# Performance work log

Measured on AMD Instinct MI355X. Metric: run time of the kernel, lower is better.

## Reference

```python
import jax, jax.numpy as jnp
import numpy as np

B, M, C, D, H, W = 2, 4, 32, 32, 32, 32
E, O = 4, 128
MC = M * C
BN_EPS = 1e-5


def setup_inputs() -> dict:
    key = jax.random.key(0)
    ks = jax.random.split(key, 8)
    inp = {
        "f0": jax.random.normal(ks[0], (B, C, D, H, W), jnp.float32),
        "f1": jax.random.normal(ks[1], (B, C, D, H, W), jnp.float32),
        "f2": jax.random.normal(ks[2], (B, C, D, H, W), jnp.float32),
        "f3": jax.random.normal(ks[3], (B, C, D, H, W), jnp.float32),
        # per-expert 1x1x1 conv weights [E, O, MC] (bias=False)
        "Wc": jax.random.normal(ks[4], (E, O, MC), jnp.float32) * 0.05,
        # BatchNorm3d params (eval mode), per expert per out-channel
        "gamma": jnp.ones((E, O), jnp.float32),
        "beta": jnp.zeros((E, O), jnp.float32),
        "rmean": jnp.zeros((E, O), jnp.float32),
        "rvar": jnp.ones((E, O), jnp.float32),
        # router Linear(MC -> E)
        "Wr": jax.random.normal(ks[5], (E, MC), jnp.float32) * 0.02,
        "br": jnp.zeros((E,), jnp.float32),
        "top_k": 2,
    }
    return inp


def reference(f0, f1, f2, f3, Wc, gamma, beta, rmean, rvar, Wr, br, top_k):
    x = jnp.concatenate([f0, f1, f2, f3], axis=1)          # [B, MC, D, H, W]
    Bn, MCn, Dn, Hn, Wn = x.shape
    En = Wr.shape[0]

    # router: global average pool -> linear -> softmax -> top-k
    pooled = x.mean(axis=(2, 3, 4))                        # [B, MC]
    logits = pooled @ Wr.T + br                            # [B, E]
    probs = jax.nn.softmax(logits, axis=-1)
    topk_vals, topk_idx = jax.lax.top_k(probs, top_k)      # [B, k]
    topk_w = topk_vals / topk_vals.sum(axis=-1, keepdims=True)

    # auxiliary load-balancing loss (top-1 one-hot)
    one_hot = jax.nn.one_hot(topk_idx[:, 0], En, dtype=probs.dtype)
    f_e = one_hot.mean(axis=0)
    p_e = probs.mean(axis=0)
    aux_loss = En * (f_e * p_e).sum()

    # all experts: 1x1x1 conv == channel GEMM, then eval-mode BN + ReLU
    xs = x.reshape(Bn, MCn, -1)                            # [B, MC, S]
    y = jnp.einsum('eoc,bcs->ebos', Wc, xs)                # [E, B, O, S]
    inv = gamma * jax.lax.rsqrt(rvar + BN_EPS)             # [E, O]
    y = y * inv[:, None, :, None] + (beta - rmean * inv)[:, None, :, None]
    y = jax.nn.relu(y)

    # dispatch/combine: per-sample expert weights scattered to [B, E]
    cw = jnp.zeros((Bn, En), x.dtype).at[
        jnp.arange(Bn)[:, None], topk_idx
    ].add(topk_w)
    out = jnp.einsum('be,ebos->bos', cw, y).reshape(Bn, -1, Dn, Hn, Wn)
    return out, aux_loss
```

## Files before the change

### kernel.cpp

```cpp
#include <hip/hip_runtime.h>
#include <stdint.h>

#define S_TOT 32768
#define MC_DIM 128
#define O_DIM 128
#define BN_EPS 1e-5f
#define S_TILE 128

#define WS_PART  0
#define WS_BIAS  512
#define WS_W2    1024

typedef __attribute__((ext_vector_type(8))) short short8;
typedef __attribute__((ext_vector_type(4))) float f32x4;

static __device__ __forceinline__ unsigned short f2bf(float f) {
    union { float f; unsigned int u; } v; v.f = f;
    unsigned int r = v.u + 0x7FFFu + ((v.u >> 16) & 1u);
    return (unsigned short)(r >> 16);
}

__global__ __launch_bounds__(256) void k_pool(
    const float* __restrict__ f0, const float* __restrict__ f1,
    const float* __restrict__ f2, const float* __restrict__ f3,
    const float* __restrict__ Wc, const float* __restrict__ gamma,
    const float* __restrict__ beta, const float* __restrict__ rmean,
    const float* __restrict__ rvar, float* __restrict__ ws) {

    __shared__ float red[4];
    int bid = blockIdx.x;
    int half = bid >> 8, ch = bid & 255;
    int b = ch >> 7, c = ch & 127;
    int t = threadIdx.x;
    int wv = t >> 6, l = t & 63;

    if (t < 32) {
        int i = bid * 32 + t;
        int eo = i >> 5;
        float inv = gamma[eo] * rsqrtf(rvar[eo] + BN_EPS);
        float4 w = ((const float4*)Wc)[i];
        uint2 pk;
        pk.x = (unsigned int)f2bf(w.x * inv) | ((unsigned int)f2bf(w.y * inv) << 16);
        pk.y = (unsigned int)f2bf(w.z * inv) | ((unsigned int)f2bf(w.w * inv) << 16);
        ((uint2*)(ws + WS_W2))[i] = pk;
    } else if (t == 32) {
        float inv = gamma[bid] * rsqrtf(rvar[bid] + BN_EPS);
        ws[WS_BIAS + bid] = beta[bid] - rmean[bid] * inv;
    }

    const float* fp = (c < 32) ? f0 : (c < 64) ? f1 : (c < 96) ? f2 : f3;
    const float4* base = (const float4*)(fp + ((size_t)b * 32 + (c & 31)) * S_TOT + half * 16384);
    float s = 0.f;
    #pragma unroll
    for (int j = 0; j < 16; ++j) {
        float4 v = base[j * 256 + t];
        s += (v.x + v.y) + (v.z + v.w);
    }
    #pragma unroll
    for (int msk = 32; msk >= 1; msk >>= 1) s += __shfl_xor(s, msk);
    if (l == 0) red[wv] = s;
    __syncthreads();
    if (t == 0) ws[WS_PART + half * 256 + ch] = (red[0] + red[1]) + (red[2] + red[3]);
}

__global__ __launch_bounds__(256, 2) void k_moe(
    const float* __restrict__ f0, const float* __restrict__ f1,
    const float* __restrict__ f2, const float* __restrict__ f3,
    const float* __restrict__ Wr, const float* __restrict__ br,
    const float* __restrict__ ws, float* __restrict__ out) {

    __shared__ uint4 tile4[2048];
    __shared__ float pooled[256];
    __shared__ int   route_e[2];
    __shared__ float route_w[2];
    char* lds = (char*)tile4;

    int bid = blockIdx.x;
    int b = bid >> 8;
    int st = bid & 255;
    int s0 = st * S_TILE;
    int t = threadIdx.x;
    int wv = t >> 6, l = t & 63;

    #pragma unroll
    for (int m = 0; m < 4; ++m) {
        const float* fp = (m == 0) ? f0 : (m == 1) ? f1 : (m == 2) ? f2 : f3;
        #pragma unroll
        for (int it = 0; it < 4; ++it) {
            int lin = it * 256 + t;
            int cql = lin >> 7;
            int sl = lin & 127;
            const float* src = fp + ((size_t)b * 32 + cql * 4) * S_TOT + s0 + sl;
            float v0 = src[0];
            float v1 = src[S_TOT];
            float v2 = src[2 * (size_t)S_TOT];
            float v3 = src[3 * (size_t)S_TOT];
            int cq = m * 8 + cql;
            int gr = cq >> 1, half = cq & 1;
            int gswz = gr ^ (sl & 15);
            int byte = sl * 256 + gswz * 16 + half * 8;
            uint2 pk;
            pk.x = (unsigned int)f2bf(v0) | ((unsigned int)f2bf(v1) << 16);
            pk.y = (unsigned int)f2bf(v2) | ((unsigned int)f2bf(v3) << 16);
            *(uint2*)(lds + byte) = pk;
        }
    }

    pooled[t] = ws[WS_PART + t] + ws[WS_PART + 256 + t];
    __syncthreads();
    if (t < 64) {
        const float s_inv = 1.0f / (float)S_TOT;
        float x0 = pooled[l] * s_inv;
        float x1 = pooled[64 + l] * s_inv;
        float y0 = pooled[128 + l] * s_inv;
        float y1 = pooled[192 + l] * s_inv;
        float lg[8];
        #pragma unroll
        for (int e = 0; e < 4; ++e) {
            float wc0 = Wr[e * MC_DIM + l];
            float wc1 = Wr[e * MC_DIM + 64 + l];
            lg[e] = x0 * wc0 + x1 * wc1;
            lg[4 + e] = y0 * wc0 + y1 * wc1;
        }
        #pragma unroll
        for (int msk = 32; msk >= 1; msk >>= 1) {
            #pragma unroll
            for (int e = 0; e < 8; ++e) lg[e] += __shfl_xor(lg[e], msk);
        }
        if (l == 0) {
            float probs[2][4];
            int top1[2];
            #pragma unroll
            for (int bb = 0; bb < 2; ++bb) {
                float lo[4];
                for (int e = 0; e < 4; ++e) lo[e] = lg[bb * 4 + e] + br[e];
                float mx = fmaxf(fmaxf(lo[0], lo[1]), fmaxf(lo[2], lo[3]));
                float sum = 0.f;
                for (int e = 0; e < 4; ++e) { probs[bb][e] = expf(lo[e] - mx); sum += probs[bb][e]; }
                for (int e = 0; e < 4; ++e) probs[bb][e] /= sum;
                int e0 = 0; float v0 = probs[bb][0];
                for (int e = 1; e < 4; ++e) if (probs[bb][e] > v0) { v0 = probs[bb][e]; e0 = e; }
                int e1 = -1; float v1 = -1.f;
                for (int e = 0; e < 4; ++e) if (e != e0 && probs[bb][e] > v1) { v1 = probs[bb][e]; e1 = e; }
                top1[bb] = e0;
                if (bb == b) {
                    float inv = 1.f / (v0 + v1);
                    route_e[0] = e0; route_e[1] = e1;
                    route_w[0] = v0 * inv; route_w[1] = v1 * inv;
                }
            }
            if (bid == 0) {
                float aux = 0.f;
                for (int e = 0; e < 4; ++e) {
                    float fe = 0.5f * ((top1[0] == e) + (top1[1] == e));
                    float pe = 0.5f * (probs[0][e] + probs[1][e]);
                    aux += fe * pe;
                }
                out[(size_t)8388608] = 4.f * aux;
            }
        }
    }
    __syncthreads();

    int e0 = route_e[0], e1 = route_e[1];
    float w0 = route_w[0], w1 = route_w[1];
    const unsigned short* W2 = (const unsigned short*)(ws + WS_W2);
    const float* bias2 = ws + WS_BIAS;

    int o0 = wv * 32;
    int lr = l & 15, lg2 = l >> 4;

    f32x4 acc[2][2][8];
    #pragma unroll
    for (int ee = 0; ee < 2; ++ee)
        #pragma unroll
        for (int of = 0; of < 2; ++of)
            #pragma unroll
            for (int sf = 0; sf < 8; ++sf)
                acc[ee][of][sf] = (f32x4){0.f, 0.f, 0.f, 0.f};

    #pragma unroll
    for (int kk = 0; kk < 4; ++kk) {
        short8 a[2][2];
        #pragma unroll
        for (int ee = 0; ee < 2; ++ee) {
            int e = ee ? e1 : e0;
            #pragma unroll
            for (int of = 0; of < 2; ++of) {
                int o = o0 + of * 16 + lr;
                a[ee][of] = *(const short8*)(W2 + ((size_t)(e * O_DIM + o) * MC_DIM + kk * 32 + lg2 * 8));
            }
        }
        #pragma unroll
        for (int sf = 0; sf < 8; ++sf) {
            int sl = sf * 16 + lr;
            int gr = kk * 4 + lg2;
            int byte = sl * 256 + ((gr ^ lr) << 4);
            short8 bb = *(const short8*)(lds + byte);
            #pragma unroll
            for (int ee = 0; ee < 2; ++ee)
                #pragma unroll
                for (int of = 0; of < 2; ++of)
                    acc[ee][of][sf] = __builtin_amdgcn_mfma_f32_16x16x32_bf16(
                        a[ee][of], bb, acc[ee][of][sf], 0, 0, 0);
        }
    }

    #pragma unroll
    for (int of = 0; of < 2; ++of) {
        #pragma unroll
        for (int r = 0; r < 4; ++r) {
            int o = o0 + of * 16 + lg2 * 4 + r;
            float bA = bias2[e0 * O_DIM + o];
            float bB = bias2[e1 * O_DIM + o];
            float* orow = out + ((size_t)(b * O_DIM + o)) * S_TOT + s0;
            #pragma unroll
            for (int sf = 0; sf < 8; ++sf) {
                float y0 = fmaxf(acc[0][of][sf][r] + bA, 0.f);
                float y1 = fmaxf(acc[1][of][sf][r] + bB, 0.f);
                orow[sf * 16 + lr] = w0 * y0 + w1 * y1;
            }
        }
    }
}

extern "C" void kernel_launch(void* const* d_in, const int* in_sizes, int n_in,
                              void* d_out, int out_size, void* d_ws, size_t ws_size,
                              hipStream_t stream) {
    const float* f0    = (const float*)d_in[0];
    const float* f1    = (const float*)d_in[1];
    const float* f2    = (const float*)d_in[2];
    const float* f3    = (const float*)d_in[3];
    const float* Wc    = (const float*)d_in[4];
    const float* gamma = (const float*)d_in[5];
    const float* beta  = (const float*)d_in[6];
    const float* rmean = (const float*)d_in[7];
    const float* rvar  = (const float*)d_in[8];
    const float* Wr    = (const float*)d_in[9];
    const float* br    = (const float*)d_in[10];
    float* ws  = (float*)d_ws;
    float* out = (float*)d_out;

    hipLaunchKernelGGL(k_pool, dim3(512), dim3(256), 0, stream,
                       f0, f1, f2, f3, Wc, gamma, beta, rmean, rvar, ws);
    hipLaunchKernelGGL(k_moe, dim3(512), dim3(256), 0, stream,
                       f0, f1, f2, f3, Wr, br, ws, out);
}
```

Before: 30.62 us.

## Compute routing redundantly per wave and halve pool grid

The pooling kernel now uses 256 blocks, each reducing a full channel instead of half, and converts twice as many weights and biases per block. The MoE kernel has every wave recompute the router logits, softmax and top-2 in registers, using shuffles, before staging its tile. This removes the shared-memory pooled buffer and one block-wide barrier that serialized routing after tile staging. The cost is redundant router math in every wave and less parallelism in the pool kernel.

Result: faster. 27.95 us, median of 2 (-8.7%).

```diff
diff --git a/kernel.cpp b/kernel.cpp
--- a/kernel.cpp
+++ b/kernel.cpp
@@ -29,13 +29,12 @@
 
     __shared__ float red[4];
     int bid = blockIdx.x;
-    int half = bid >> 8, ch = bid & 255;
-    int b = ch >> 7, c = ch & 127;
+    int b = bid >> 7, c = bid & 127;
     int t = threadIdx.x;
     int wv = t >> 6, l = t & 63;
 
-    if (t < 32) {
-        int i = bid * 32 + t;
+    if (t < 64) {
+        int i = bid * 64 + t;
         int eo = i >> 5;
         float inv = gamma[eo] * rsqrtf(rvar[eo] + BN_EPS);
         float4 w = ((const float4*)Wc)[i];
@@ -43,16 +42,17 @@
         pk.x = (unsigned int)f2bf(w.x * inv) | ((unsigned int)f2bf(w.y * inv) << 16);
         pk.y = (unsigned int)f2bf(w.z * inv) | ((unsigned int)f2bf(w.w * inv) << 16);
         ((uint2*)(ws + WS_W2))[i] = pk;
-    } else if (t == 32) {
-        float inv = gamma[bid] * rsqrtf(rvar[bid] + BN_EPS);
-        ws[WS_BIAS + bid] = beta[bid] - rmean[bid] * inv;
+    } else if (t < 66) {
+        int i = bid * 2 + (t - 64);
+        float inv = gamma[i] * rsqrtf(rvar[i] + BN_EPS);
+        ws[WS_BIAS + i] = beta[i] - rmean[i] * inv;
     }
 
     const float* fp = (c < 32) ? f0 : (c < 64) ? f1 : (c < 96) ? f2 : f3;
-    const float4* base = (const float4*)(fp + ((size_t)b * 32 + (c & 31)) * S_TOT + half * 16384);
+    const float4* base = (const float4*)(fp + ((size_t)b * 32 + (c & 31)) * S_TOT);
     float s = 0.f;
     #pragma unroll
-    for (int j = 0; j < 16; ++j) {
+    for (int j = 0; j < 32; ++j) {
         float4 v = base[j * 256 + t];
         s += (v.x + v.y) + (v.z + v.w);
     }
@@ -60,7 +60,7 @@
     for (int msk = 32; msk >= 1; msk >>= 1) s += __shfl_xor(s, msk);
     if (l == 0) red[wv] = s;
     __syncthreads();
-    if (t == 0) ws[WS_PART + half * 256 + ch] = (red[0] + red[1]) + (red[2] + red[3]);
+    if (t == 0) ws[WS_PART + bid] = (red[0] + red[1]) + (red[2] + red[3]);
 }
 
 __global__ __launch_bounds__(256, 2) void k_moe(
@@ -70,9 +70,6 @@
     const float* __restrict__ ws, float* __restrict__ out) {
 
     __shared__ uint4 tile4[2048];
-    __shared__ float pooled[256];
-    __shared__ int   route_e[2];
-    __shared__ float route_w[2];
     char* lds = (char*)tile4;
 
     int bid = blockIdx.x;
@@ -81,6 +78,68 @@
     int s0 = st * S_TILE;
     int t = threadIdx.x;
     int wv = t >> 6, l = t & 63;
+
+    float lg[8];
+    {
+        float p0 = ws[WS_PART + l];
+        float p1 = ws[WS_PART + 64 + l];
+        float p2 = ws[WS_PART + 128 + l];
+        float p3 = ws[WS_PART + 192 + l];
+        #pragma unroll
+        for (int e = 0; e < 4; ++e) {
+            float wc0 = Wr[e * MC_DIM + l];
+            float wc1 = Wr[e * MC_DIM + 64 + l];
+            lg[e]     = p0 * wc0 + p1 * wc1;
+            lg[4 + e] = p2 * wc0 + p3 * wc1;
+        }
+        #pragma unroll
+        for (int msk = 32; msk >= 1; msk >>= 1) {
+            #pragma unroll
+            for (int e = 0; e < 8; ++e) lg[e] += __shfl_xor(lg[e], msk);
+        }
+    }
+    int e0, e1;
+    float w0, w1;
+    {
+        const float s_inv = 1.0f / (float)S_TOT;
+        float probs[2][4];
+        int top1[2];
+        int ee0[2], ee1[2];
+        float vv0[2], vv1[2];
+        #pragma unroll
+        for (int bb = 0; bb < 2; ++bb) {
+            float lo[4];
+            #pragma unroll
+            for (int e = 0; e < 4; ++e) lo[e] = lg[bb * 4 + e] * s_inv + br[e];
+            float mx = fmaxf(fmaxf(lo[0], lo[1]), fmaxf(lo[2], lo[3]));
+            float sum = 0.f;
+            #pragma unroll
+            for (int e = 0; e < 4; ++e) { probs[bb][e] = __expf(lo[e] - mx); sum += probs[bb][e]; }
+            float rs = 1.f / sum;
+            #pragma unroll
+            for (int e = 0; e < 4; ++e) probs[bb][e] *= rs;
+            int a0 = 0; float m0 = probs[bb][0];
+            #pragma unroll
+            for (int e = 1; e < 4; ++e) if (probs[bb][e] > m0) { m0 = probs[bb][e]; a0 = e; }
+            int a1 = -1; float m1 = -1.f;
+            #pragma unroll
+            for (int e = 0; e < 4; ++e) if (e != a0 && probs[bb][e] > m1) { m1 = probs[bb][e]; a1 = e; }
+            top1[bb] = a0; ee0[bb] = a0; ee1[bb] = a1; vv0[bb] = m0; vv1[bb] = m1;
+        }
+        float inv = 1.f / (vv0[b] + vv1[b]);
+        e0 = ee0[b]; e1 = ee1[b];
+        w0 = vv0[b] * inv; w1 = vv1[b] * inv;
+        if (bid == 0 && t == 0) {
+            float aux = 0.f;
+            #pragma unroll
+            for (int e = 0; e < 4; ++e) {
+                float fe = 0.5f * ((top1[0] == e) + (top1[1] == e));
+                float pe = 0.5f * (probs[0][e] + probs[1][e]);
+                aux += fe * pe;
+            }
+            out[(size_t)8388608] = 4.f * aux;
+        }
+    }
 
     #pragma unroll
     for (int m = 0; m < 4; ++m) {
@@ -105,65 +164,8 @@
             *(uint2*)(lds + byte) = pk;
         }
     }
-
-    pooled[t] = ws[WS_PART + t] + ws[WS_PART + 256 + t];
     __syncthreads();
-    if (t < 64) {
-        const float s_inv = 1.0f / (float)S_TOT;
-        float x0 = pooled[l] * s_inv;
-        float x1 = pooled[64 + l] * s_inv;
-        float y0 = pooled[128 + l] * s_inv;
-        float y1 = pooled[192 + l] * s_inv;
-        float lg[8];
-        #pragma unroll
-        for (int e = 0; e < 4; ++e) {
-            float wc0 = Wr[e * MC_DIM + l];
-            float wc1 = Wr[e * MC_DIM + 64 + l];
-            lg[e] = x0 * wc0 + x1 * wc1;
-            lg[4 + e] = y0 * wc0 + y1 * wc1;
-        }
-        #pragma unroll
-        for (int msk = 32; msk >= 1; msk >>= 1) {
-            #pragma unroll
-            for (int e = 0; e < 8; ++e) lg[e] += __shfl_xor(lg[e], msk);
-        }
-        if (l == 0) {
-            float probs[2][4];
-            int top1[2];
-            #pragma unroll
-            for (int bb = 0; bb < 2; ++bb) {
-                float lo[4];
-                for (int e = 0; e < 4; ++e) lo[e] = lg[bb * 4 + e] + br[e];
-                float mx = fmaxf(fmaxf(lo[0], lo[1]), fmaxf(lo[2], lo[3]));
-                float sum = 0.f;
-                for (int e = 0; e < 4; ++e) { probs[bb][e] = expf(lo[e] - mx); sum += probs[bb][e]; }
-                for (int e = 0; e < 4; ++e) probs[bb][e] /= sum;
-                int e0 = 0; float v0 = probs[bb][0];
-                for (int e = 1; e < 4; ++e) if (probs[bb][e] > v0) { v0 = probs[bb][e]; e0 = e; }
-                int e1 = -1; float v1 = -1.f;
-                for (int e = 0; e < 4; ++e) if (e != e0 && probs[bb][e] > v1) { v1 = probs[bb][e]; e1 = e; }
-                top1[bb] = e0;
-                if (bb == b) {
-                    float inv = 1.f / (v0 + v1);
-                    route_e[0] = e0; route_e[1] = e1;
-                    route_w[0] = v0 * inv; route_w[1] = v1 * inv;
-                }
-            }
-            if (bid == 0) {
-                float aux = 0.f;
-                for (int e = 0; e < 4; ++e) {
-                    float fe = 0.5f * ((top1[0] == e) + (top1[1] == e));
-                    float pe = 0.5f * (probs[0][e] + probs[1][e]);
-                    aux += fe * pe;
-                }
-                out[(size_t)8388608] = 4.f * aux;
-            }
-        }
-    }
-    __syncthreads();
-
-    int e0 = route_e[0], e1 = route_e[1];
-    float w0 = route_w[0], w1 = route_w[1];
+
     const unsigned short* W2 = (const unsigned short*)(ws + WS_W2);
     const float* bias2 = ws + WS_BIAS;
 
@@ -241,7 +243,7 @@
     float* ws  = (float*)d_ws;
     float* out = (float*)d_out;
 
-    hipLaunchKernelGGL(k_pool, dim3(512), dim3(256), 0, stream,
+    hipLaunchKernelGGL(k_pool, dim3(256), dim3(256), 0, stream,
                        f0, f1, f2, f3, Wc, gamma, beta, rmean, rvar, ws);
     hipLaunchKernelGGL(k_moe, dim3(512), dim3(256), 0, stream,
                        f0, f1, f2, f3, Wr, br, ws, out);
```
